# Performance work log

Hardware: AMD Instinct MI355X
Metric: run time of the kernel (lower is better)

Reference implementation:

```python
import jax, jax.numpy as jnp
import numpy as np
from jax import lax

BATCH, SEQ_LEN, HIDDEN, CLASSES = 512, 256, 1024, 128

def _xavier(key, shape):
    fan_out, fan_in = shape
    std = float(np.sqrt(2.0 / (fan_in + fan_out)))
    return jax.random.normal(key, shape, dtype=jnp.float32) * std

def setup_inputs() -> dict:
    key = jax.random.key(0)
    k_x, k_hx, k_hh, k_ph = jax.random.split(key, 4)
    return {
        "x": jax.random.normal(k_x, (BATCH, SEQ_LEN), dtype=jnp.float32),
        "W_hx": _xavier(k_hx, (HIDDEN, 1)),
        "W_hh": _xavier(k_hh, (HIDDEN, HIDDEN)),
        "b_h": jnp.zeros((HIDDEN,), dtype=jnp.float32),
        "W_ph": _xavier(k_ph, (CLASSES, HIDDEN)),
        "b_p": jnp.zeros((CLASSES,), dtype=jnp.float32),
    }

def reference(x, W_hx, W_hh, b_h, W_ph, b_p):
    # x: [B, T] (input_dim == 1 per timestep, as in the torch module)
    B = x.shape[0]
    H = W_hh.shape[0]
    h0 = jnp.zeros((B, H), dtype=x.dtype)

    def step(h, xt):
        # xt: [B]; xt[:, None] @ W_hx.T -> [B, H]
        h_new = jnp.tanh(xt[:, None] @ W_hx.T + h @ W_hh.T + b_h)
        return h_new, None

    h_last, _ = lax.scan(step, h0, x.T)  # scan over time: x.T is [T, B]
    # Output head applied to final hidden state (loop's last p in torch code)
    return h_last @ W_ph.T + b_p  # [B, num_classes]
```

## Files before the change

### kernel.cpp

```cpp
#include <hip/hip_runtime.h>
#include <stdint.h>


#define BATCH 512
#define SEQ   256
#define HID   1024
#define CLS   128

#define GB 16
#define GJ 16
#define BT 32
#define JT 64
#define WSTR 1028
#define SSTR 1032
#define HSTR 72
#define SMEM_BYTES (JT * WSTR * 2)
#define SS_BYTES   (BT * SSTR * 2)
#define RB_OFF     SS_BYTES
#define HS_OFF     (RB_OFF + 8192)
#define HBUF_HALVES (BATCH * HID)

typedef __attribute__((ext_vector_type(8))) short  bf16x8;
typedef __attribute__((ext_vector_type(4))) short  s16x4;
typedef __attribute__((ext_vector_type(4))) float  f32x4;
typedef __attribute__((ext_vector_type(4))) int    i32x4;
typedef __attribute__((ext_vector_type(2))) unsigned int u32x2;

__device__ __forceinline__ unsigned short f2bf(float f) {
  unsigned int u = __float_as_uint(f);
  u = (u + 0x7FFFu + ((u >> 16) & 1u)) >> 16;
  return (unsigned short)u;
}
__device__ __forceinline__ float b2f(short h) {
  return __uint_as_float(((unsigned int)(unsigned short)h) << 16);
}

__device__ __forceinline__ void store_flag(int* p, int v) {
  asm volatile("global_store_dword %0, %1, off sc0 sc1" :: "v"(p), "v"(v) : "memory");
}
__device__ __forceinline__ int load_flag(const int* p) {
  int v;
  asm volatile("global_load_dword %0, %1, off sc0 sc1\n\t"
               "s_waitcnt vmcnt(0)" : "=v"(v) : "v"(p) : "memory");
  return v;
}
__device__ __forceinline__ void store16(void* p, i32x4 v) {
  asm volatile("global_store_dwordx4 %0, %1, off sc0 sc1" :: "v"(p), "v"(v) : "memory");
}
__device__ __forceinline__ void waitcnt0() {
  asm volatile("s_waitcnt vmcnt(0)" ::: "memory");
}
__device__ __forceinline__ void barrier_lgkm() {
  asm volatile("s_waitcnt lgkmcnt(0)\n\ts_barrier" ::: "memory");
}
__device__ __forceinline__ void issue4(const void* p, i32x4& a, i32x4& b, i32x4& c, i32x4& d) {
  asm volatile(
    "global_load_dwordx4 %0, %4, off sc0 sc1\n\t"
    "global_load_dwordx4 %1, %4, off offset:128 sc0 sc1\n\t"
    "global_load_dwordx4 %2, %4, off offset:256 sc0 sc1\n\t"
    "global_load_dwordx4 %3, %4, off offset:384 sc0 sc1"
    : "=&v"(a), "=&v"(b), "=&v"(c), "=&v"(d)
    : "v"(p) : "memory");
}
#define DEF_WAIT(NAME, N) \
__device__ __forceinline__ void NAME(i32x4& a, i32x4& b, i32x4& c, i32x4& d) { \
  asm volatile("s_waitcnt vmcnt(" #N ")" : "+v"(a), "+v"(b), "+v"(c), "+v"(d) :: "memory"); \
}
DEF_WAIT(wait_vm12, 12)
DEF_WAIT(wait_vm8, 8)
DEF_WAIT(wait_vm4, 4)
DEF_WAIT(wait_vm0, 0)

__device__ __forceinline__ void wr16(short* p, i32x4 v) {
  union { i32x4 i; bf16x8 v8; } u; u.i = v;
  *(bf16x8*)p = u.v8;
}
__device__ __forceinline__ bf16x8 ld8_64(const short* p) {
  union { bf16x8 v8; s16x4 h[2]; } u;
  u.h[0] = *(const s16x4*)p;
  u.h[1] = *(const s16x4*)(p + 4);
  return u.v8;
}
__device__ __forceinline__ float tanh_fast(float z) {
  float e = __expf(2.f * z);
  return 1.f - 2.f / (e + 1.f);
}

template<int CK>
__device__ __forceinline__ void mfma_chunk(const short* sA0, const bf16x8 (&fB)[2][16],
                                           f32x4 (&acc)[2][2]) {
#pragma unroll
  for (int ks = 0; ks < 8; ++ks) {
    const int kk = CK * 8 + ks;
    bf16x8 a0 = *(const bf16x8*)(sA0 + CK * 256 + ks * 32);
    bf16x8 a1 = *(const bf16x8*)(sA0 + 16 * SSTR + CK * 256 + ks * 32);
#pragma unroll
    for (int nt = 0; nt < 2; ++nt) {
      acc[0][nt] = __builtin_amdgcn_mfma_f32_16x16x32_bf16(a0, fB[nt][kk], acc[0][nt], 0, 0, 0);
      acc[1][nt] = __builtin_amdgcn_mfma_f32_16x16x32_bf16(a1, fB[nt][kk], acc[1][nt], 0, 0, 0);
    }
  }
}

__global__ void __launch_bounds__(256, 1)
rnn_persistent(const float* __restrict__ x, const float* __restrict__ Whx,
               const float* __restrict__ Whh, const float* __restrict__ bh,
               const float* __restrict__ Wph, const float* __restrict__ bp,
               float* __restrict__ out, unsigned short* hbuf, int* flags)
{
  extern __shared__ short smem[];
  short* sW   = smem;
  short* sS   = smem;
  float* rbuf = (float*)((char*)smem + RB_OFF);
  short* hS   = (short*)((char*)smem + HS_OFF);

  const int tid  = threadIdx.x;
  const int bg   = blockIdx.x & 15;
  const int jg   = blockIdx.x >> 4;
  const int lane = tid & 63;
  const int wv   = tid >> 6;
  const int l15  = lane & 15;
  const int quad = lane >> 4;
  const int npair = wv & 1;
  const int khalf = wv >> 1;

  {
    const int jr = tid >> 2;
    const int kq = tid & 3;
    const float* src = Whh + (jg * JT + jr) * HID + kq * 256;
    short* dst = sW + jr * WSTR + kq * 256;
#pragma unroll 4
    for (int i = 0; i < 64; ++i) {
      float4 f = *(const float4*)(src + i * 4);
      s16x4 h4;
      h4.x = (short)f2bf(f.x); h4.y = (short)f2bf(f.y);
      h4.z = (short)f2bf(f.z); h4.w = (short)f2bf(f.w);
      *(s16x4*)(dst + i * 4) = h4;
    }
  }
  __syncthreads();

  bf16x8 fB[2][16];
#pragma unroll
  for (int nt = 0; nt < 2; ++nt) {
    const short* bp_ = sW + (npair * 32 + nt * 16 + l15) * WSTR + khalf * 512 + quad * 8;
#pragma unroll
    for (int kk = 0; kk < 16; ++kk)
      fB[nt][kk] = ld8_64(bp_ + kk * 32);
  }
  __syncthreads();

  const int jbase = jg * JT + npair * 32;
  const float whx0 = Whx[jbase + l15];
  const float whx1 = Whx[jbase + 16 + l15];
  const float bh0  = bh[jbase + l15];
  const float bh1  = bh[jbase + 16 + l15];

  const int sr  = tid >> 3;
  const int seg = tid & 7;

  int* myflags = flags + bg * 64;

  const short* sA0 = sS + l15 * SSTR + khalf * 512 + quad * 8;

  for (int t = 0; t < SEQ; ++t) {
    const unsigned short* hin = hbuf + ((t + 1) & 1) * HBUF_HALVES;
    unsigned short*      hout = hbuf + (t & 1) * HBUF_HALVES;

    f32x4 acc[2][2];
#pragma unroll
    for (int mt = 0; mt < 2; ++mt)
#pragma unroll
      for (int nt = 0; nt < 2; ++nt)
        acc[mt][nt] = (f32x4){0.f, 0.f, 0.f, 0.f};

    float xv[2][4];
    {
      const float* xp = x + (bg * BT + quad * 4) * SEQ + t;
#pragma unroll
      for (int r = 0; r < 4; ++r) {
        xv[0][r] = xp[r * SEQ];
        xv[1][r] = xp[(16 + r) * SEQ];
      }
    }

    if (t > 0) {
      if (tid < GJ) {
        while (load_flag(myflags + tid) < t) {}
      }
      __syncthreads();

      const char* lbase = (const char*)(hin + (bg * BT + sr) * HID) + seg * 16;
      short* sdst = sS + sr * SSTR + seg * 8;

      i32x4 a0, a1, a2, a3, b0, b1, b2, b3, c0, c1, c2, c3, d0, d1, d2, d3;
      issue4(lbase,        a0, a1, a2, a3);
      issue4(lbase + 512,  b0, b1, b2, b3);
      issue4(lbase + 1024, c0, c1, c2, c3);
      issue4(lbase + 1536, d0, d1, d2, d3);

      wait_vm12(a0, a1, a2, a3);
      wr16(sdst, a0); wr16(sdst + 64, a1); wr16(sdst + 128, a2); wr16(sdst + 192, a3);
      barrier_lgkm();
      if (khalf == 0) mfma_chunk<0>(sA0, fB, acc);

      wait_vm8(b0, b1, b2, b3);
      wr16(sdst + 256, b0); wr16(sdst + 320, b1); wr16(sdst + 384, b2); wr16(sdst + 448, b3);
      barrier_lgkm();
      if (khalf == 0) mfma_chunk<1>(sA0, fB, acc);

      wait_vm4(c0, c1, c2, c3);
      wr16(sdst + 512, c0); wr16(sdst + 576, c1); wr16(sdst + 640, c2); wr16(sdst + 704, c3);
      barrier_lgkm();
      if (khalf == 1) mfma_chunk<0>(sA0, fB, acc);

      wait_vm0(d0, d1, d2, d3);
      wr16(sdst + 768, d0); wr16(sdst + 832, d1); wr16(sdst + 896, d2); wr16(sdst + 960, d3);
      barrier_lgkm();
      if (khalf == 1) mfma_chunk<1>(sA0, fB, acc);
    }

    if (khalf == 1) {
#pragma unroll
      for (int mt = 0; mt < 2; ++mt)
#pragma unroll
        for (int nt = 0; nt < 2; ++nt)
          *(f32x4*)(rbuf + ((npair * 4 + mt * 2 + nt) * 64 + lane) * 4) = acc[mt][nt];
    }
    barrier_lgkm();

    if (khalf == 0) {
#pragma unroll
      for (int mt = 0; mt < 2; ++mt)
#pragma unroll
        for (int nt = 0; nt < 2; ++nt) {
          f32x4 p = *(const f32x4*)(rbuf + ((npair * 4 + mt * 2 + nt) * 64 + lane) * 4);
          acc[mt][nt] += p;
        }
#pragma unroll
      for (int mt = 0; mt < 2; ++mt) {
#pragma unroll
        for (int r = 0; r < 4; ++r) {
          const int row = mt * 16 + quad * 4 + r;
          float z0 = acc[mt][0][r] + xv[mt][r] * whx0 + bh0;
          hS[row * HSTR + npair * 32 + l15] = (short)f2bf(tanh_fast(z0));
          float z1 = acc[mt][1][r] + xv[mt][r] * whx1 + bh1;
          hS[row * HSTR + npair * 32 + 16 + l15] = (short)f2bf(tanh_fast(z1));
        }
      }
    }
    barrier_lgkm();

    {
      union { bf16x8 v8; i32x4 i; } u;
      u.v8 = *(const bf16x8*)(hS + sr * HSTR + seg * 8);
      unsigned short* dst = hout + (bg * BT + sr) * HID + jg * JT + seg * 8;
      store16(dst, u.i);
    }
    waitcnt0();
    barrier_lgkm();
    if (tid == 0) store_flag(myflags + jg, t + 1);
  }

  if (tid < GJ) {
    while (load_flag(myflags + tid) < SEQ) {}
  }
  __syncthreads();

  const unsigned short* hlast = hbuf + ((SEQ - 1) & 1) * HBUF_HALVES;
  {
    const char* lbase = (const char*)(hlast + (bg * BT + sr) * HID) + seg * 16;
    short* sdst = sS + sr * SSTR + seg * 8;
    i32x4 p0, p1, p2, p3;
#pragma unroll
    for (int c = 0; c < 4; ++c) {
      issue4(lbase + c * 512, p0, p1, p2, p3);
      waitcnt0();
      wr16(sdst + c * 256, p0); wr16(sdst + c * 256 + 64, p1);
      wr16(sdst + c * 256 + 128, p2); wr16(sdst + c * 256 + 192, p3);
    }
  }
  __syncthreads();

  const int cc = tid & 7;
  const int cg = jg * 8 + cc;
  const int hr = tid >> 3;
  float acc = 0.f;
  const float* wp = Wph + cg * HID;
  const short* hs = sS + hr * SSTR;
#pragma unroll 8
  for (int k4 = 0; k4 < 256; ++k4) {
    float4 w  = *(const float4*)(wp + k4 * 4);
    s16x4 hv  = *(const s16x4*)(hs + k4 * 4);
    acc += b2f(hv.x) * w.x + b2f(hv.y) * w.y + b2f(hv.z) * w.z + b2f(hv.w) * w.w;
  }
  out[(bg * BT + hr) * CLS + cg] = acc + bp[cg];
}

extern "C" void kernel_launch(void* const* d_in, const int* in_sizes, int n_in,
                              void* d_out, int out_size, void* d_ws, size_t ws_size,
                              hipStream_t stream) {
  const float* x   = (const float*)d_in[0];
  const float* Whx = (const float*)d_in[1];
  const float* Whh = (const float*)d_in[2];
  const float* bh  = (const float*)d_in[3];
  const float* Wph = (const float*)d_in[4];
  const float* bp  = (const float*)d_in[5];
  float* out = (float*)d_out;

  unsigned short* hbuf = (unsigned short*)d_ws;
  int* flags = (int*)((char*)d_ws + (size_t)2 * HBUF_HALVES * 2);

  hipFuncSetAttribute(reinterpret_cast<const void*>(rnn_persistent),
                      hipFuncAttributeMaxDynamicSharedMemorySize, SMEM_BYTES);

  rnn_persistent<<<dim3(GB * GJ), dim3(256), SMEM_BYTES, stream>>>(
      x, Whx, Whh, bh, Wph, bp, out, hbuf, flags);
}
```

Before: 1.147 ms.

## Split batch tile into two half-groups with ping-pong flags to overlap sync

Each block now processes two 16-row batch slices per timestep, A and B, each with its own flag array. While one slice's hidden state is being published and waited on, the other slice's matmul runs, which hides part of the inter-block barrier latency. Operand loads now go straight from global memory into MFMA registers instead of staging through LDS. Flag polling uses a single lane with vectorized min over 16 flags. The cost is more complex dependency ordering and two barriers per half-step.

```diff
diff --git a/kernel.cpp b/kernel.cpp
--- a/kernel.cpp
+++ b/kernel.cpp
@@ -9,22 +9,23 @@
 
 #define GB 16
 #define GJ 16
-#define BT 32
+#define BT 16
 #define JT 64
 #define WSTR 1028
-#define SSTR 1032
 #define HSTR 72
+#define HDSTR 1032
 #define SMEM_BYTES (JT * WSTR * 2)
-#define SS_BYTES   (BT * SSTR * 2)
-#define RB_OFF     SS_BYTES
-#define HS_OFF     (RB_OFF + 8192)
+#define RBA_OFF 0
+#define RBB_OFF 4096
+#define HSA_OFF 8192
+#define HSB_OFF 12288
+#define HEAD_OFF 16384
 #define HBUF_HALVES (BATCH * HID)
 
 typedef __attribute__((ext_vector_type(8))) short  bf16x8;
 typedef __attribute__((ext_vector_type(4))) short  s16x4;
 typedef __attribute__((ext_vector_type(4))) float  f32x4;
 typedef __attribute__((ext_vector_type(4))) int    i32x4;
-typedef __attribute__((ext_vector_type(2))) unsigned int u32x2;
 
 __device__ __forceinline__ unsigned short f2bf(float f) {
   unsigned int u = __float_as_uint(f);
@@ -38,12 +39,6 @@
 __device__ __forceinline__ void store_flag(int* p, int v) {
   asm volatile("global_store_dword %0, %1, off sc0 sc1" :: "v"(p), "v"(v) : "memory");
 }
-__device__ __forceinline__ int load_flag(const int* p) {
-  int v;
-  asm volatile("global_load_dword %0, %1, off sc0 sc1\n\t"
-               "s_waitcnt vmcnt(0)" : "=v"(v) : "v"(p) : "memory");
-  return v;
-}
 __device__ __forceinline__ void store16(void* p, i32x4 v) {
   asm volatile("global_store_dwordx4 %0, %1, off sc0 sc1" :: "v"(p), "v"(v) : "memory");
 }
@@ -53,12 +48,21 @@
 __device__ __forceinline__ void barrier_lgkm() {
   asm volatile("s_waitcnt lgkmcnt(0)\n\ts_barrier" ::: "memory");
 }
-__device__ __forceinline__ void issue4(const void* p, i32x4& a, i32x4& b, i32x4& c, i32x4& d) {
+__device__ __forceinline__ void issue4s(const void* p, i32x4& a, i32x4& b, i32x4& c, i32x4& d) {
   asm volatile(
     "global_load_dwordx4 %0, %4, off sc0 sc1\n\t"
-    "global_load_dwordx4 %1, %4, off offset:128 sc0 sc1\n\t"
-    "global_load_dwordx4 %2, %4, off offset:256 sc0 sc1\n\t"
-    "global_load_dwordx4 %3, %4, off offset:384 sc0 sc1"
+    "global_load_dwordx4 %1, %4, off offset:64 sc0 sc1\n\t"
+    "global_load_dwordx4 %2, %4, off offset:128 sc0 sc1\n\t"
+    "global_load_dwordx4 %3, %4, off offset:192 sc0 sc1"
+    : "=&v"(a), "=&v"(b), "=&v"(c), "=&v"(d)
+    : "v"(p) : "memory");
+}
+__device__ __forceinline__ void issue4c(const void* p, i32x4& a, i32x4& b, i32x4& c, i32x4& d) {
+  asm volatile(
+    "global_load_dwordx4 %0, %4, off sc0 sc1\n\t"
+    "global_load_dwordx4 %1, %4, off offset:16 sc0 sc1\n\t"
+    "global_load_dwordx4 %2, %4, off offset:32 sc0 sc1\n\t"
+    "global_load_dwordx4 %3, %4, off offset:48 sc0 sc1"
     : "=&v"(a), "=&v"(b), "=&v"(c), "=&v"(d)
     : "v"(p) : "memory");
 }
@@ -71,48 +75,54 @@
 DEF_WAIT(wait_vm4, 4)
 DEF_WAIT(wait_vm0, 0)
 
-__device__ __forceinline__ void wr16(short* p, i32x4 v) {
-  union { i32x4 i; bf16x8 v8; } u; u.i = v;
-  *(bf16x8*)p = u.v8;
-}
-__device__ __forceinline__ bf16x8 ld8_64(const short* p) {
-  union { bf16x8 v8; s16x4 h[2]; } u;
-  u.h[0] = *(const s16x4*)p;
-  u.h[1] = *(const s16x4*)(p + 4);
-  return u.v8;
-}
+__device__ __forceinline__ int flags_min16(const int* p) {
+  i32x4 f0, f1, f2, f3;
+  asm volatile(
+    "global_load_dwordx4 %0, %4, off sc0 sc1\n\t"
+    "global_load_dwordx4 %1, %4, off offset:16 sc0 sc1\n\t"
+    "global_load_dwordx4 %2, %4, off offset:32 sc0 sc1\n\t"
+    "global_load_dwordx4 %3, %4, off offset:48 sc0 sc1\n\t"
+    "s_waitcnt vmcnt(0)"
+    : "=&v"(f0), "=&v"(f1), "=&v"(f2), "=&v"(f3) : "v"(p) : "memory");
+  int m = f0.x;
+  m = f0.y < m ? f0.y : m;  m = f0.z < m ? f0.z : m;  m = f0.w < m ? f0.w : m;
+  m = f1.x < m ? f1.x : m;  m = f1.y < m ? f1.y : m;  m = f1.z < m ? f1.z : m;  m = f1.w < m ? f1.w : m;
+  m = f2.x < m ? f2.x : m;  m = f2.y < m ? f2.y : m;  m = f2.z < m ? f2.z : m;  m = f2.w < m ? f2.w : m;
+  m = f3.x < m ? f3.x : m;  m = f3.y < m ? f3.y : m;  m = f3.z < m ? f3.z : m;  m = f3.w < m ? f3.w : m;
+  return m;
+}
+__device__ __forceinline__ void wave_spin(const int* p, int t, int lane) {
+  if (lane == 0) {
+    while (flags_min16(p) < t) {}
+  }
+}
+
 __device__ __forceinline__ float tanh_fast(float z) {
   float e = __expf(2.f * z);
   return 1.f - 2.f / (e + 1.f);
 }
 
-template<int CK>
-__device__ __forceinline__ void mfma_chunk(const short* sA0, const bf16x8 (&fB)[2][16],
-                                           f32x4 (&acc)[2][2]) {
-#pragma unroll
-  for (int ks = 0; ks < 8; ++ks) {
-    const int kk = CK * 8 + ks;
-    bf16x8 a0 = *(const bf16x8*)(sA0 + CK * 256 + ks * 32);
-    bf16x8 a1 = *(const bf16x8*)(sA0 + 16 * SSTR + CK * 256 + ks * 32);
-#pragma unroll
-    for (int nt = 0; nt < 2; ++nt) {
-      acc[0][nt] = __builtin_amdgcn_mfma_f32_16x16x32_bf16(a0, fB[nt][kk], acc[0][nt], 0, 0, 0);
-      acc[1][nt] = __builtin_amdgcn_mfma_f32_16x16x32_bf16(a1, fB[nt][kk], acc[1][nt], 0, 0, 0);
-    }
-  }
+__device__ __forceinline__ void mfma2(i32x4 av, bf16x8 fb0, bf16x8 fb1,
+                                      f32x4& acc0, f32x4& acc1) {
+  union { i32x4 i; bf16x8 v8; } u; u.i = av;
+  acc0 = __builtin_amdgcn_mfma_f32_16x16x32_bf16(u.v8, fb0, acc0, 0, 0, 0);
+  acc1 = __builtin_amdgcn_mfma_f32_16x16x32_bf16(u.v8, fb1, acc1, 0, 0, 0);
 }
 
 __global__ void __launch_bounds__(256, 1)
 rnn_persistent(const float* __restrict__ x, const float* __restrict__ Whx,
                const float* __restrict__ Whh, const float* __restrict__ bh,
                const float* __restrict__ Wph, const float* __restrict__ bp,
-               float* __restrict__ out, unsigned short* hbuf, int* flags)
+               float* __restrict__ out, unsigned short* hbuf,
+               int* flagsA, int* flagsB)
 {
   extern __shared__ short smem[];
   short* sW   = smem;
-  short* sS   = smem;
-  float* rbuf = (float*)((char*)smem + RB_OFF);
-  short* hS   = (short*)((char*)smem + HS_OFF);
+  float* rbA  = (float*)((char*)smem + RBA_OFF);
+  float* rbB  = (float*)((char*)smem + RBB_OFF);
+  short* hSA  = (short*)((char*)smem + HSA_OFF);
+  short* hSB  = (short*)((char*)smem + HSB_OFF);
+  short* hd   = (short*)((char*)smem + HEAD_OFF);
 
   const int tid  = threadIdx.x;
   const int bg   = blockIdx.x & 15;
@@ -145,156 +155,201 @@
   for (int nt = 0; nt < 2; ++nt) {
     const short* bp_ = sW + (npair * 32 + nt * 16 + l15) * WSTR + khalf * 512 + quad * 8;
 #pragma unroll
-    for (int kk = 0; kk < 16; ++kk)
-      fB[nt][kk] = ld8_64(bp_ + kk * 32);
+    for (int kk = 0; kk < 16; ++kk) {
+      union { bf16x8 v8; s16x4 h[2]; } u;
+      u.h[0] = *(const s16x4*)(bp_ + kk * 32);
+      u.h[1] = *(const s16x4*)(bp_ + kk * 32 + 4);
+      fB[nt][kk] = u.v8;
+    }
   }
   __syncthreads();
 
-  const int jbase = jg * JT + npair * 32;
-  const float whx0 = Whx[jbase + l15];
-  const float whx1 = Whx[jbase + 16 + l15];
-  const float bh0  = bh[jbase + l15];
-  const float bh1  = bh[jbase + 16 + l15];
-
-  const int sr  = tid >> 3;
-  const int seg = tid & 7;
-
-  int* myflags = flags + bg * 64;
-
-  const short* sA0 = sS + l15 * SSTR + khalf * 512 + quad * 8;
+  const int jb0 = jg * JT + npair * 32;
+  const float whx0 = Whx[jb0 + l15];
+  const float whx1 = Whx[jb0 + 16 + l15];
+  const float bh0  = bh[jb0 + l15];
+  const float bh1  = bh[jb0 + 16 + l15];
+
+  const int browA = bg * BT;
+  const int browB = 256 + bg * BT;
+
+  int* mfA = flagsA + bg * 16;
+  int* mfB = flagsB + bg * 16;
 
   for (int t = 0; t < SEQ; ++t) {
     const unsigned short* hin = hbuf + ((t + 1) & 1) * HBUF_HALVES;
     unsigned short*      hout = hbuf + (t & 1) * HBUF_HALVES;
 
-    f32x4 acc[2][2];
-#pragma unroll
-    for (int mt = 0; mt < 2; ++mt)
-#pragma unroll
-      for (int nt = 0; nt < 2; ++nt)
-        acc[mt][nt] = (f32x4){0.f, 0.f, 0.f, 0.f};
-
-    float xv[2][4];
-    {
-      const float* xp = x + (bg * BT + quad * 4) * SEQ + t;
+    float xv[4];
+    if (khalf == 0) {
+      const float* xp = x + (browA + quad * 4) * SEQ + t;
+#pragma unroll
+      for (int r = 0; r < 4; ++r) xv[r] = xp[r * SEQ];
+    }
+    f32x4 acc0 = {0.f, 0.f, 0.f, 0.f};
+    f32x4 acc1 = {0.f, 0.f, 0.f, 0.f};
+
+    if (t > 0) {
+      const char* ab = (const char*)(hin + (browA + l15) * HID + khalf * 512 + quad * 8);
+      i32x4 a0,a1,a2,a3, b0,b1,b2,b3, c0,c1,c2,c3, d0,d1,d2,d3;
+      issue4s(ab,       a0,a1,a2,a3);
+      issue4s(ab + 256, b0,b1,b2,b3);
+      issue4s(ab + 512, c0,c1,c2,c3);
+      issue4s(ab + 768, d0,d1,d2,d3);
+      wait_vm12(a0,a1,a2,a3);
+      mfma2(a0, fB[0][0],  fB[1][0],  acc0, acc1);
+      mfma2(a1, fB[0][1],  fB[1][1],  acc0, acc1);
+      mfma2(a2, fB[0][2],  fB[1][2],  acc0, acc1);
+      mfma2(a3, fB[0][3],  fB[1][3],  acc0, acc1);
+      wait_vm8(b0,b1,b2,b3);
+      mfma2(b0, fB[0][4],  fB[1][4],  acc0, acc1);
+      mfma2(b1, fB[0][5],  fB[1][5],  acc0, acc1);
+      mfma2(b2, fB[0][6],  fB[1][6],  acc0, acc1);
+      mfma2(b3, fB[0][7],  fB[1][7],  acc0, acc1);
+      wait_vm4(c0,c1,c2,c3);
+      mfma2(c0, fB[0][8],  fB[1][8],  acc0, acc1);
+      mfma2(c1, fB[0][9],  fB[1][9],  acc0, acc1);
+      mfma2(c2, fB[0][10], fB[1][10], acc0, acc1);
+      mfma2(c3, fB[0][11], fB[1][11], acc0, acc1);
+      wait_vm0(d0,d1,d2,d3);
+      mfma2(d0, fB[0][12], fB[1][12], acc0, acc1);
+      mfma2(d1, fB[0][13], fB[1][13], acc0, acc1);
+      mfma2(d2, fB[0][14], fB[1][14], acc0, acc1);
+      mfma2(d3, fB[0][15], fB[1][15], acc0, acc1);
+    }
+    if (khalf == 1) {
+      *(f32x4*)(rbA + ((npair * 2 + 0) * 64 + lane) * 4) = acc0;
+      *(f32x4*)(rbA + ((npair * 2 + 1) * 64 + lane) * 4) = acc1;
+    }
+    barrier_lgkm();
+    if (khalf == 0) {
+      f32x4 p0 = *(const f32x4*)(rbA + ((npair * 2 + 0) * 64 + lane) * 4);
+      f32x4 p1 = *(const f32x4*)(rbA + ((npair * 2 + 1) * 64 + lane) * 4);
+      acc0 += p0; acc1 += p1;
 #pragma unroll
       for (int r = 0; r < 4; ++r) {
-        xv[0][r] = xp[r * SEQ];
-        xv[1][r] = xp[(16 + r) * SEQ];
+        const int row = quad * 4 + r;
+        hSA[row * HSTR + npair * 32 + l15]      = (short)f2bf(tanh_fast(acc0[r] + xv[r] * whx0 + bh0));
+        hSA[row * HSTR + npair * 32 + 16 + l15] = (short)f2bf(tanh_fast(acc1[r] + xv[r] * whx1 + bh1));
       }
     }
+    barrier_lgkm();
+    if (tid < 128) {
+      union { bf16x8 v8; i32x4 i; } u;
+      u.v8 = *(const bf16x8*)(hSA + (tid >> 3) * HSTR + (tid & 7) * 8);
+      store16(hout + (browA + (tid >> 3)) * HID + jg * JT + (tid & 7) * 8, u.i);
+    }
+    if (t > 0) wave_spin(mfB, t, lane);
+    else       waitcnt0();
+    barrier_lgkm();
+    if (tid == 0) store_flag(mfA + jg, t + 1);
+
+    if (khalf == 0) {
+      const float* xp = x + (browB + quad * 4) * SEQ + t;
+#pragma unroll
+      for (int r = 0; r < 4; ++r) xv[r] = xp[r * SEQ];
+    }
+    acc0 = (f32x4){0.f, 0.f, 0.f, 0.f};
+    acc1 = (f32x4){0.f, 0.f, 0.f, 0.f};
 
     if (t > 0) {
-      if (tid < GJ) {
-        while (load_flag(myflags + tid) < t) {}
+      const char* ab = (const char*)(hin + (browB + l15) * HID + khalf * 512 + quad * 8);
+      i32x4 a0,a1,a2,a3, b0,b1,b2,b3, c0,c1,c2,c3, d0,d1,d2,d3;
+      issue4s(ab,       a0,a1,a2,a3);
+      issue4s(ab + 256, b0,b1,b2,b3);
+      issue4s(ab + 512, c0,c1,c2,c3);
+      issue4s(ab + 768, d0,d1,d2,d3);
+      wait_vm12(a0,a1,a2,a3);
+      mfma2(a0, fB[0][0],  fB[1][0],  acc0, acc1);
+      mfma2(a1, fB[0][1],  fB[1][1],  acc0, acc1);
+      mfma2(a2, fB[0][2],  fB[1][2],  acc0, acc1);
+      mfma2(a3, fB[0][3],  fB[1][3],  acc0, acc1);
+      wait_vm8(b0,b1,b2,b3);
+      mfma2(b0, fB[0][4],  fB[1][4],  acc0, acc1);
+      mfma2(b1, fB[0][5],  fB[1][5],  acc0, acc1);
+      mfma2(b2, fB[0][6],  fB[1][6],  acc0, acc1);
+      mfma2(b3, fB[0][7],  fB[1][7],  acc0, acc1);
+      wait_vm4(c0,c1,c2,c3);
+      mfma2(c0, fB[0][8],  fB[1][8],  acc0, acc1);
+      mfma2(c1, fB[0][9],  fB[1][9],  acc0, acc1);
+      mfma2(c2, fB[0][10], fB[1][10], acc0, acc1);
+      mfma2(c3, fB[0][11], fB[1][11], acc0, acc1);
+      wait_vm0(d0,d1,d2,d3);
+      mfma2(d0, fB[0][12], fB[1][12], acc0, acc1);
+      mfma2(d1, fB[0][13], fB[1][13], acc0, acc1);
+      mfma2(d2, fB[0][14], fB[1][14], acc0, acc1);
+      mfma2(d3, fB[0][15], fB[1][15], acc0, acc1);
+    }
+    if (khalf == 1) {
+      *(f32x4*)(rbB + ((npair * 2 + 0) * 64 + lane) * 4) = acc0;
+      *(f32x4*)(rbB + ((npair * 2 + 1) * 64 + lane) * 4) = acc1;
+    }
+    barrier_lgkm();
+    if (khalf == 0) {
+      f32x4 p0 = *(const f32x4*)(rbB + ((npair * 2 + 0) * 64 + lane) * 4);
+      f32x4 p1 = *(const f32x4*)(rbB + ((npair * 2 + 1) * 64 + lane) * 4);
+      acc0 += p0; acc1 += p1;
+#pragma unroll
+      for (int r = 0; r < 4; ++r) {
+        const int row = quad * 4 + r;
+        hSB[row * HSTR + npair * 32 + l15]      = (short)f2bf(tanh_fast(acc0[r] + xv[r] * whx0 + bh0));
+        hSB[row * HSTR + npair * 32 + 16 + l15] = (short)f2bf(tanh_fast(acc1[r] + xv[r] * whx1 + bh1));
       }
-      __syncthreads();
-
-      const char* lbase = (const char*)(hin + (bg * BT + sr) * HID) + seg * 16;
-      short* sdst = sS + sr * SSTR + seg * 8;
-
-      i32x4 a0, a1, a2, a3, b0, b1, b2, b3, c0, c1, c2, c3, d0, d1, d2, d3;
-      issue4(lbase,        a0, a1, a2, a3);
-      issue4(lbase + 512,  b0, b1, b2, b3);
-      issue4(lbase + 1024, c0, c1, c2, c3);
-      issue4(lbase + 1536, d0, d1, d2, d3);
-
-      wait_vm12(a0, a1, a2, a3);
-      wr16(sdst, a0); wr16(sdst + 64, a1); wr16(sdst + 128, a2); wr16(sdst + 192, a3);
-      barrier_lgkm();
-      if (khalf == 0) mfma_chunk<0>(sA0, fB, acc);
-
-      wait_vm8(b0, b1, b2, b3);
-      wr16(sdst + 256, b0); wr16(sdst + 320, b1); wr16(sdst + 384, b2); wr16(sdst + 448, b3);
-      barrier_lgkm();
-      if (khalf == 0) mfma_chunk<1>(sA0, fB, acc);
-
-      wait_vm4(c0, c1, c2, c3);
-      wr16(sdst + 512, c0); wr16(sdst + 576, c1); wr16(sdst + 640, c2); wr16(sdst + 704, c3);
-      barrier_lgkm();
-      if (khalf == 1) mfma_chunk<0>(sA0, fB, acc);
-
-      wait_vm0(d0, d1, d2, d3);
-      wr16(sdst + 768, d0); wr16(sdst + 832, d1); wr16(sdst + 896, d2); wr16(sdst + 960, d3);
-      barrier_lgkm();
-      if (khalf == 1) mfma_chunk<1>(sA0, fB, acc);
-    }
-
-    if (khalf == 1) {
-#pragma unroll
-      for (int mt = 0; mt < 2; ++mt)
-#pragma unroll
-        for (int nt = 0; nt < 2; ++nt)
-          *(f32x4*)(rbuf + ((npair * 4 + mt * 2 + nt) * 64 + lane) * 4) = acc[mt][nt];
-    }
-    barrier_lgkm();
-
-    if (khalf == 0) {
-#pragma unroll
-      for (int mt = 0; mt < 2; ++mt)
-#pragma unroll
-        for (int nt = 0; nt < 2; ++nt) {
-          f32x4 p = *(const f32x4*)(rbuf + ((npair * 4 + mt * 2 + nt) * 64 + lane) * 4);
-          acc[mt][nt] += p;
-        }
-#pragma unroll
-      for (int mt = 0; mt < 2; ++mt) {
-#pragma unroll
-        for (int r = 0; r < 4; ++r) {
-          const int row = mt * 16 + quad * 4 + r;
-          float z0 = acc[mt][0][r] + xv[mt][r] * whx0 + bh0;
-          hS[row * HSTR + npair * 32 + l15] = (short)f2bf(tanh_fast(z0));
-          float z1 = acc[mt][1][r] + xv[mt][r] * whx1 + bh1;
-          hS[row * HSTR + npair * 32 + 16 + l15] = (short)f2bf(tanh_fast(z1));
-        }
-      }
-    }
-    barrier_lgkm();
-
-    {
+    }
+    barrier_lgkm();
+    if (tid < 128) {
       union { bf16x8 v8; i32x4 i; } u;
-      u.v8 = *(const bf16x8*)(hS + sr * HSTR + seg * 8);
-      unsigned short* dst = hout + (bg * BT + sr) * HID + jg * JT + seg * 8;
-      store16(dst, u.i);
-    }
-    waitcnt0();
-    barrier_lgkm();
-    if (tid == 0) store_flag(myflags + jg, t + 1);
-  }
-
-  if (tid < GJ) {
-    while (load_flag(myflags + tid) < SEQ) {}
-  }
-  __syncthreads();
+      u.v8 = *(const bf16x8*)(hSB + (tid >> 3) * HSTR + (tid & 7) * 8);
+      store16(hout + (browB + (tid >> 3)) * HID + jg * JT + (tid & 7) * 8, u.i);
+    }
+    wave_spin(mfA, t + 1, lane);
+    barrier_lgkm();
+    if (tid == 0) store_flag(mfB + jg, t + 1);
+  }
+
+  wave_spin(mfB, SEQ, lane);
+  barrier_lgkm();
 
   const unsigned short* hlast = hbuf + ((SEQ - 1) & 1) * HBUF_HALVES;
   {
-    const char* lbase = (const char*)(hlast + (bg * BT + sr) * HID) + seg * 16;
-    short* sdst = sS + sr * SSTR + seg * 8;
-    i32x4 p0, p1, p2, p3;
-#pragma unroll
-    for (int c = 0; c < 4; ++c) {
-      issue4(lbase + c * 512, p0, p1, p2, p3);
-      waitcnt0();
-      wr16(sdst + c * 256, p0); wr16(sdst + c * 256 + 64, p1);
-      wr16(sdst + c * 256 + 128, p2); wr16(sdst + c * 256 + 192, p3);
-    }
+    const int ri  = tid >> 3;
+    const int seg = tid & 7;
+    const int grow = (ri < 16) ? (browA + ri) : (browB + ri - 16);
+    const char* pb = (const char*)(hlast + grow * HID + seg * 128);
+    i32x4 p0,p1,p2,p3, q0,q1,q2,q3, r0,r1,r2,r3, s0,s1,s2,s3;
+    issue4c(pb,       p0,p1,p2,p3);
+    issue4c(pb + 64,  q0,q1,q2,q3);
+    issue4c(pb + 128, r0,r1,r2,r3);
+    issue4c(pb + 192, s0,s1,s2,s3);
+    waitcnt0();
+    short* d = hd + ri * HDSTR + seg * 128;
+    union { i32x4 i; bf16x8 v8; } u;
+    u.i = p0; *(bf16x8*)(d)      = u.v8;  u.i = p1; *(bf16x8*)(d + 8)  = u.v8;
+    u.i = p2; *(bf16x8*)(d + 16) = u.v8;  u.i = p3; *(bf16x8*)(d + 24) = u.v8;
+    u.i = q0; *(bf16x8*)(d + 32) = u.v8;  u.i = q1; *(bf16x8*)(d + 40) = u.v8;
+    u.i = q2; *(bf16x8*)(d + 48) = u.v8;  u.i = q3; *(bf16x8*)(d + 56) = u.v8;
+    u.i = r0; *(bf16x8*)(d + 64) = u.v8;  u.i = r1; *(bf16x8*)(d + 72) = u.v8;
+    u.i = r2; *(bf16x8*)(d + 80) = u.v8;  u.i = r3; *(bf16x8*)(d + 88) = u.v8;
+    u.i = s0; *(bf16x8*)(d + 96) = u.v8;  u.i = s1; *(bf16x8*)(d + 104) = u.v8;
+    u.i = s2; *(bf16x8*)(d + 112) = u.v8; u.i = s3; *(bf16x8*)(d + 120) = u.v8;
   }
   __syncthreads();
-
-  const int cc = tid & 7;
-  const int cg = jg * 8 + cc;
-  const int hr = tid >> 3;
-  float acc = 0.f;
-  const float* wp = Wph + cg * HID;
-  const short* hs = sS + hr * SSTR;
+  {
+    const int ri = tid >> 3;
+    const int cc = tid & 7;
+    const int cg = jg * 8 + cc;
+    const int grow = (ri < 16) ? (browA + ri) : (browB + ri - 16);
+    const float* wp = Wph + cg * HID;
+    const short* hs = hd + ri * HDSTR;
+    float acc = 0.f;
 #pragma unroll 8
-  for (int k4 = 0; k4 < 256; ++k4) {
-    float4 w  = *(const float4*)(wp + k4 * 4);
-    s16x4 hv  = *(const s16x4*)(hs + k4 * 4);
-    acc += b2f(hv.x) * w.x + b2f(hv.y) * w.y + b2f(hv.z) * w.z + b2f(hv.w) * w.w;
-  }
-  out[(bg * BT + hr) * CLS + cg] = acc + bp[cg];
+    for (int k4 = 0; k4 < 256; ++k4) {
+      float4 w = *(const float4*)(wp + k4 * 4);
+      s16x4 hv = *(const s16x4*)(hs + k4 * 4);
+      acc += b2f(hv.x) * w.x + b2f(hv.y) * w.y + b2f(hv.z) * w.z + b2f(hv.w) * w.w;
+    }
+    out[grow * CLS + cg] = acc + bp[cg];
+  }
 }
 
 extern "C" void kernel_launch(void* const* d_in, const int* in_sizes, int n_in,
@@ -309,11 +364,12 @@
   float* out = (float*)d_out;
 
   unsigned short* hbuf = (unsigned short*)d_ws;
-  int* flags = (int*)((char*)d_ws + (size_t)2 * HBUF_HALVES * 2);
+  int* flagsA = (int*)((char*)d_ws + (size_t)2 * HBUF_HALVES * 2);
+  int* flagsB = flagsA + 16 * 16;
 
   hipFuncSetAttribute(reinterpret_cast<const void*>(rnn_persistent),
                       hipFuncAttributeMaxDynamicSharedMemorySize, SMEM_BYTES);
 
   rnn_persistent<<<dim3(GB * GJ), dim3(256), SMEM_BYTES, stream>>>(
-      x, Whx, Whh, bh, Wph, bp, out, hbuf, flags);
-}
+      x, Whx, Whh, bh, Wph, bp, out, hbuf, flagsA, flagsB);
+}
```

After: 1.822 ms. +58.9%, slower.

## Use XCD-local cache scope for h exchange when a batch group shares one XCD

Applied to the files above, without the earlier changes.

At startup each block publishes its XCC_ID, and the blocks of a batch group check whether they all run on the same XCD. If they do, the hidden-state exchange and flag polling use sc0-only (L2-scope) loads and stores instead of sc0 sc1 system-coherent ones, which should cut the round-trip latency per timestep. Flag polling also changes from 16 threads polling one flag each to one thread reading all 16 flags with vector loads and taking the minimum, with a bounded fallback to the coherent path. This adds a startup handshake, and the fast path only runs if the hardware places a group's blocks on one XCD.

```diff
diff --git a/kernel.cpp b/kernel.cpp
--- a/kernel.cpp
+++ b/kernel.cpp
@@ -24,7 +24,6 @@
 typedef __attribute__((ext_vector_type(4))) short  s16x4;
 typedef __attribute__((ext_vector_type(4))) float  f32x4;
 typedef __attribute__((ext_vector_type(4))) int    i32x4;
-typedef __attribute__((ext_vector_type(2))) unsigned int u32x2;
 
 __device__ __forceinline__ unsigned short f2bf(float f) {
   unsigned int u = __float_as_uint(f);
@@ -35,32 +34,86 @@
   return __uint_as_float(((unsigned int)(unsigned short)h) << 16);
 }
 
-__device__ __forceinline__ void store_flag(int* p, int v) {
+template<bool LP>
+__device__ __forceinline__ void g_store_flag(int* p, int v) {
+  if constexpr (LP)
+    asm volatile("global_store_dword %0, %1, off sc0" :: "v"(p), "v"(v) : "memory");
+  else
+    asm volatile("global_store_dword %0, %1, off sc0 sc1" :: "v"(p), "v"(v) : "memory");
+}
+template<bool LP>
+__device__ __forceinline__ void g_store16(void* p, i32x4 v) {
+  if constexpr (LP)
+    asm volatile("global_store_dwordx4 %0, %1, off sc0" :: "v"(p), "v"(v) : "memory");
+  else
+    asm volatile("global_store_dwordx4 %0, %1, off sc0 sc1" :: "v"(p), "v"(v) : "memory");
+}
+template<bool LP>
+__device__ __forceinline__ void g_issue4(const void* p, i32x4& a, i32x4& b, i32x4& c, i32x4& d) {
+  if constexpr (LP)
+    asm volatile(
+      "global_load_dwordx4 %0, %4, off sc0\n\t"
+      "global_load_dwordx4 %1, %4, off offset:128 sc0\n\t"
+      "global_load_dwordx4 %2, %4, off offset:256 sc0\n\t"
+      "global_load_dwordx4 %3, %4, off offset:384 sc0"
+      : "=&v"(a), "=&v"(b), "=&v"(c), "=&v"(d) : "v"(p) : "memory");
+  else
+    asm volatile(
+      "global_load_dwordx4 %0, %4, off sc0 sc1\n\t"
+      "global_load_dwordx4 %1, %4, off offset:128 sc0 sc1\n\t"
+      "global_load_dwordx4 %2, %4, off offset:256 sc0 sc1\n\t"
+      "global_load_dwordx4 %3, %4, off offset:384 sc0 sc1"
+      : "=&v"(a), "=&v"(b), "=&v"(c), "=&v"(d) : "v"(p) : "memory");
+}
+template<bool LP>
+__device__ __forceinline__ int flags_min16(const int* p) {
+  i32x4 f0, f1, f2, f3;
+  if constexpr (LP)
+    asm volatile(
+      "global_load_dwordx4 %0, %4, off sc0\n\t"
+      "global_load_dwordx4 %1, %4, off offset:16 sc0\n\t"
+      "global_load_dwordx4 %2, %4, off offset:32 sc0\n\t"
+      "global_load_dwordx4 %3, %4, off offset:48 sc0\n\t"
+      "s_waitcnt vmcnt(0)"
+      : "=&v"(f0), "=&v"(f1), "=&v"(f2), "=&v"(f3) : "v"(p) : "memory");
+  else
+    asm volatile(
+      "global_load_dwordx4 %0, %4, off sc0 sc1\n\t"
+      "global_load_dwordx4 %1, %4, off offset:16 sc0 sc1\n\t"
+      "global_load_dwordx4 %2, %4, off offset:32 sc0 sc1\n\t"
+      "global_load_dwordx4 %3, %4, off offset:48 sc0 sc1\n\t"
+      "s_waitcnt vmcnt(0)"
+      : "=&v"(f0), "=&v"(f1), "=&v"(f2), "=&v"(f3) : "v"(p) : "memory");
+  int m = f0.x;
+  m = f0.y < m ? f0.y : m;  m = f0.z < m ? f0.z : m;  m = f0.w < m ? f0.w : m;
+  m = f1.x < m ? f1.x : m;  m = f1.y < m ? f1.y : m;  m = f1.z < m ? f1.z : m;  m = f1.w < m ? f1.w : m;
+  m = f2.x < m ? f2.x : m;  m = f2.y < m ? f2.y : m;  m = f2.z < m ? f2.z : m;  m = f2.w < m ? f2.w : m;
+  m = f3.x < m ? f3.x : m;  m = f3.y < m ? f3.y : m;  m = f3.z < m ? f3.z : m;  m = f3.w < m ? f3.w : m;
+  return m;
+}
+__device__ __forceinline__ void flags_minmax16_dev(const int* p, int& mn, int& mx) {
+  i32x4 f0, f1, f2, f3;
+  asm volatile(
+    "global_load_dwordx4 %0, %4, off sc0 sc1\n\t"
+    "global_load_dwordx4 %1, %4, off offset:16 sc0 sc1\n\t"
+    "global_load_dwordx4 %2, %4, off offset:32 sc0 sc1\n\t"
+    "global_load_dwordx4 %3, %4, off offset:48 sc0 sc1\n\t"
+    "s_waitcnt vmcnt(0)"
+    : "=&v"(f0), "=&v"(f1), "=&v"(f2), "=&v"(f3) : "v"(p) : "memory");
+  int a[16] = {f0.x,f0.y,f0.z,f0.w, f1.x,f1.y,f1.z,f1.w,
+               f2.x,f2.y,f2.z,f2.w, f3.x,f3.y,f3.z,f3.w};
+  mn = a[0]; mx = a[0];
+#pragma unroll
+  for (int i = 1; i < 16; ++i) { mn = a[i] < mn ? a[i] : mn; mx = a[i] > mx ? a[i] : mx; }
+}
+__device__ __forceinline__ void store_flag_dev(int* p, int v) {
   asm volatile("global_store_dword %0, %1, off sc0 sc1" :: "v"(p), "v"(v) : "memory");
-}
-__device__ __forceinline__ int load_flag(const int* p) {
-  int v;
-  asm volatile("global_load_dword %0, %1, off sc0 sc1\n\t"
-               "s_waitcnt vmcnt(0)" : "=v"(v) : "v"(p) : "memory");
-  return v;
-}
-__device__ __forceinline__ void store16(void* p, i32x4 v) {
-  asm volatile("global_store_dwordx4 %0, %1, off sc0 sc1" :: "v"(p), "v"(v) : "memory");
 }
 __device__ __forceinline__ void waitcnt0() {
   asm volatile("s_waitcnt vmcnt(0)" ::: "memory");
 }
 __device__ __forceinline__ void barrier_lgkm() {
   asm volatile("s_waitcnt lgkmcnt(0)\n\ts_barrier" ::: "memory");
-}
-__device__ __forceinline__ void issue4(const void* p, i32x4& a, i32x4& b, i32x4& c, i32x4& d) {
-  asm volatile(
-    "global_load_dwordx4 %0, %4, off sc0 sc1\n\t"
-    "global_load_dwordx4 %1, %4, off offset:128 sc0 sc1\n\t"
-    "global_load_dwordx4 %2, %4, off offset:256 sc0 sc1\n\t"
-    "global_load_dwordx4 %3, %4, off offset:384 sc0 sc1"
-    : "=&v"(a), "=&v"(b), "=&v"(c), "=&v"(d)
-    : "v"(p) : "memory");
 }
 #define DEF_WAIT(NAME, N) \
 __device__ __forceinline__ void NAME(i32x4& a, i32x4& b, i32x4& c, i32x4& d) { \
@@ -75,12 +128,6 @@
   union { i32x4 i; bf16x8 v8; } u; u.i = v;
   *(bf16x8*)p = u.v8;
 }
-__device__ __forceinline__ bf16x8 ld8_64(const short* p) {
-  union { bf16x8 v8; s16x4 h[2]; } u;
-  u.h[0] = *(const s16x4*)p;
-  u.h[1] = *(const s16x4*)(p + 4);
-  return u.v8;
-}
 __device__ __forceinline__ float tanh_fast(float z) {
   float e = __expf(2.f * z);
   return 1.f - 2.f / (e + 1.f);
@@ -99,6 +146,164 @@
       acc[0][nt] = __builtin_amdgcn_mfma_f32_16x16x32_bf16(a0, fB[nt][kk], acc[0][nt], 0, 0, 0);
       acc[1][nt] = __builtin_amdgcn_mfma_f32_16x16x32_bf16(a1, fB[nt][kk], acc[1][nt], 0, 0, 0);
     }
+  }
+}
+
+template<bool LP>
+__device__ __forceinline__ void spin_flags(const int* myflags, int t) {
+  if constexpr (LP) {
+    int tries = 0;
+    for (;;) {
+      if (flags_min16<true>(myflags) >= t) return;
+      if (++tries >= 64) break;
+    }
+    while (flags_min16<false>(myflags) < t) {}
+  } else {
+    while (flags_min16<false>(myflags) < t) {}
+  }
+}
+
+template<bool LP>
+__device__ __forceinline__ void rnn_body(
+    const float* __restrict__ x, const float* __restrict__ Wph,
+    const float* __restrict__ bp, float* __restrict__ out,
+    unsigned short* hbuf, int* myflags,
+    short* sS, float* rbuf, short* hS,
+    const bf16x8 (&fB)[2][16],
+    int tid, int bg, int jg, int lane, int npair, int khalf,
+    int l15, int quad,
+    float whx0, float whx1, float bh0, float bh1,
+    int sr, int seg)
+{
+  const short* sA0 = sS + l15 * SSTR + khalf * 512 + quad * 8;
+
+  for (int t = 0; t < SEQ; ++t) {
+    const unsigned short* hin = hbuf + ((t + 1) & 1) * HBUF_HALVES;
+    unsigned short*      hout = hbuf + (t & 1) * HBUF_HALVES;
+
+    f32x4 acc[2][2];
+#pragma unroll
+    for (int mt = 0; mt < 2; ++mt)
+#pragma unroll
+      for (int nt = 0; nt < 2; ++nt)
+        acc[mt][nt] = (f32x4){0.f, 0.f, 0.f, 0.f};
+
+    float xv[2][4];
+    {
+      const float* xp = x + (bg * BT + quad * 4) * SEQ + t;
+#pragma unroll
+      for (int r = 0; r < 4; ++r) {
+        xv[0][r] = xp[r * SEQ];
+        xv[1][r] = xp[(16 + r) * SEQ];
+      }
+    }
+
+    if (t > 0) {
+      if (tid == 0) spin_flags<LP>(myflags, t);
+      __syncthreads();
+
+      const char* lbase = (const char*)(hin + (bg * BT + sr) * HID) + seg * 16;
+      short* sdst = sS + sr * SSTR + seg * 8;
+
+      i32x4 a0, a1, a2, a3, b0, b1, b2, b3, c0, c1, c2, c3, d0, d1, d2, d3;
+      g_issue4<LP>(lbase,        a0, a1, a2, a3);
+      g_issue4<LP>(lbase + 512,  b0, b1, b2, b3);
+      g_issue4<LP>(lbase + 1024, c0, c1, c2, c3);
+      g_issue4<LP>(lbase + 1536, d0, d1, d2, d3);
+
+      wait_vm12(a0, a1, a2, a3);
+      wr16(sdst, a0); wr16(sdst + 64, a1); wr16(sdst + 128, a2); wr16(sdst + 192, a3);
+      barrier_lgkm();
+      if (khalf == 0) mfma_chunk<0>(sA0, fB, acc);
+
+      wait_vm8(b0, b1, b2, b3);
+      wr16(sdst + 256, b0); wr16(sdst + 320, b1); wr16(sdst + 384, b2); wr16(sdst + 448, b3);
+      barrier_lgkm();
+      if (khalf == 0) mfma_chunk<1>(sA0, fB, acc);
+
+      wait_vm4(c0, c1, c2, c3);
+      wr16(sdst + 512, c0); wr16(sdst + 576, c1); wr16(sdst + 640, c2); wr16(sdst + 704, c3);
+      barrier_lgkm();
+      if (khalf == 1) mfma_chunk<0>(sA0, fB, acc);
+
+      wait_vm0(d0, d1, d2, d3);
+      wr16(sdst + 768, d0); wr16(sdst + 832, d1); wr16(sdst + 896, d2); wr16(sdst + 960, d3);
+      barrier_lgkm();
+      if (khalf == 1) mfma_chunk<1>(sA0, fB, acc);
+    }
+
+    if (khalf == 1) {
+#pragma unroll
+      for (int mt = 0; mt < 2; ++mt)
+#pragma unroll
+        for (int nt = 0; nt < 2; ++nt)
+          *(f32x4*)(rbuf + ((npair * 4 + mt * 2 + nt) * 64 + lane) * 4) = acc[mt][nt];
+    }
+    barrier_lgkm();
+
+    if (khalf == 0) {
+#pragma unroll
+      for (int mt = 0; mt < 2; ++mt)
+#pragma unroll
+        for (int nt = 0; nt < 2; ++nt) {
+          f32x4 p = *(const f32x4*)(rbuf + ((npair * 4 + mt * 2 + nt) * 64 + lane) * 4);
+          acc[mt][nt] += p;
+        }
+#pragma unroll
+      for (int mt = 0; mt < 2; ++mt) {
+#pragma unroll
+        for (int r = 0; r < 4; ++r) {
+          const int row = mt * 16 + quad * 4 + r;
+          float z0 = acc[mt][0][r] + xv[mt][r] * whx0 + bh0;
+          hS[row * HSTR + npair * 32 + l15] = (short)f2bf(tanh_fast(z0));
+          float z1 = acc[mt][1][r] + xv[mt][r] * whx1 + bh1;
+          hS[row * HSTR + npair * 32 + 16 + l15] = (short)f2bf(tanh_fast(z1));
+        }
+      }
+    }
+    barrier_lgkm();
+
+    {
+      union { bf16x8 v8; i32x4 i; } u;
+      u.v8 = *(const bf16x8*)(hS + sr * HSTR + seg * 8);
+      g_store16<LP>(hout + (bg * BT + sr) * HID + jg * JT + seg * 8, u.i);
+    }
+    waitcnt0();
+    barrier_lgkm();
+    if (tid == 0) g_store_flag<LP>(myflags + jg, t + 1);
+  }
+
+  if (tid == 0) spin_flags<LP>(myflags, SEQ);
+  __syncthreads();
+
+  const unsigned short* hlast = hbuf + ((SEQ - 1) & 1) * HBUF_HALVES;
+  {
+    const char* lbase = (const char*)(hlast + (bg * BT + sr) * HID) + seg * 16;
+    short* sdst = sS + sr * SSTR + seg * 8;
+    i32x4 p0, p1, p2, p3;
+#pragma unroll
+    for (int c = 0; c < 4; ++c) {
+      g_issue4<LP>(lbase + c * 512, p0, p1, p2, p3);
+      waitcnt0();
+      wr16(sdst + c * 256, p0); wr16(sdst + c * 256 + 64, p1);
+      wr16(sdst + c * 256 + 128, p2); wr16(sdst + c * 256 + 192, p3);
+    }
+  }
+  __syncthreads();
+
+  {
+    const int cg = jg * 8 + (tid & 7);
+    const int hr = tid >> 3;
+    float acc = 0.f;
+    const float* wp = Wph + cg * HID;
+    const short* hs = sS + hr * SSTR;
+#pragma unroll 8
+    for (int k4 = 0; k4 < 256; ++k4) {
+      float4 w  = *(const float4*)(wp + k4 * 4);
+      s16x4 hv  = *(const s16x4*)(hs + k4 * 4);
+      acc += b2f(hv.x) * w.x + b2f(hv.y) * w.y + b2f(hv.z) * w.z + b2f(hv.w) * w.w;
+    }
+    out[(bg * BT + hr) * CLS + cg] = acc + bp[cg];
   }
 }
 
@@ -113,6 +318,7 @@
   short* sS   = smem;
   float* rbuf = (float*)((char*)smem + RB_OFF);
   short* hS   = (short*)((char*)smem + HS_OFF);
+  __shared__ int s_local;
 
   const int tid  = threadIdx.x;
   const int bg   = blockIdx.x & 15;
@@ -123,6 +329,15 @@
   const int quad = lane >> 4;
   const int npair = wv & 1;
   const int khalf = wv >> 1;
+
+  int* myflags = flags + bg * 64;
+  int* xline   = myflags + 16;
+
+  if (tid == 0) {
+    int xcd;
+    asm volatile("s_getreg_b32 %0, hwreg(HW_REG_XCC_ID)" : "=s"(xcd));
+    store_flag_dev(xline + jg, 4096 + xcd);
+  }
 
   {
     const int jr = tid >> 2;
@@ -145,156 +360,38 @@
   for (int nt = 0; nt < 2; ++nt) {
     const short* bp_ = sW + (npair * 32 + nt * 16 + l15) * WSTR + khalf * 512 + quad * 8;
 #pragma unroll
-    for (int kk = 0; kk < 16; ++kk)
-      fB[nt][kk] = ld8_64(bp_ + kk * 32);
+    for (int kk = 0; kk < 16; ++kk) {
+      union { bf16x8 v8; s16x4 h[2]; } u;
+      u.h[0] = *(const s16x4*)(bp_ + kk * 32);
+      u.h[1] = *(const s16x4*)(bp_ + kk * 32 + 4);
+      fB[nt][kk] = u.v8;
+    }
+  }
+
+  if (tid == 0) {
+    int mn, mx;
+    do { flags_minmax16_dev(xline, mn, mx); } while (mn < 4096);
+    s_local = (mn == mx) ? 1 : 0;
   }
   __syncthreads();
-
-  const int jbase = jg * JT + npair * 32;
-  const float whx0 = Whx[jbase + l15];
-  const float whx1 = Whx[jbase + 16 + l15];
-  const float bh0  = bh[jbase + l15];
-  const float bh1  = bh[jbase + 16 + l15];
-
+  const bool local = (s_local != 0);
+
+  const int jb0 = jg * JT + npair * 32;
+  const float whx0 = Whx[jb0 + l15];
+  const float whx1 = Whx[jb0 + 16 + l15];
+  const float bh0  = bh[jb0 + l15];
+  const float bh1  = bh[jb0 + 16 + l15];
   const int sr  = tid >> 3;
   const int seg = tid & 7;
 
-  int* myflags = flags + bg * 64;
-
-  const short* sA0 = sS + l15 * SSTR + khalf * 512 + quad * 8;
-
-  for (int t = 0; t < SEQ; ++t) {
-    const unsigned short* hin = hbuf + ((t + 1) & 1) * HBUF_HALVES;
-    unsigned short*      hout = hbuf + (t & 1) * HBUF_HALVES;
-
-    f32x4 acc[2][2];
-#pragma unroll
-    for (int mt = 0; mt < 2; ++mt)
-#pragma unroll
-      for (int nt = 0; nt < 2; ++nt)
-        acc[mt][nt] = (f32x4){0.f, 0.f, 0.f, 0.f};
-
-    float xv[2][4];
-    {
-      const float* xp = x + (bg * BT + quad * 4) * SEQ + t;
-#pragma unroll
-      for (int r = 0; r < 4; ++r) {
-        xv[0][r] = xp[r * SEQ];
-        xv[1][r] = xp[(16 + r) * SEQ];
-      }
-    }
-
-    if (t > 0) {
-      if (tid < GJ) {
-        while (load_flag(myflags + tid) < t) {}
-      }
-      __syncthreads();
-
-      const char* lbase = (const char*)(hin + (bg * BT + sr) * HID) + seg * 16;
-      short* sdst = sS + sr * SSTR + seg * 8;
-
-      i32x4 a0, a1, a2, a3, b0, b1, b2, b3, c0, c1, c2, c3, d0, d1, d2, d3;
-      issue4(lbase,        a0, a1, a2, a3);
-      issue4(lbase + 512,  b0, b1, b2, b3);
-      issue4(lbase + 1024, c0, c1, c2, c3);
-      issue4(lbase + 1536, d0, d1, d2, d3);
-
-      wait_vm12(a0, a1, a2, a3);
-      wr16(sdst, a0); wr16(sdst + 64, a1); wr16(sdst + 128, a2); wr16(sdst + 192, a3);
-      barrier_lgkm();
-      if (khalf == 0) mfma_chunk<0>(sA0, fB, acc);
-
-      wait_vm8(b0, b1, b2, b3);
-      wr16(sdst + 256, b0); wr16(sdst + 320, b1); wr16(sdst + 384, b2); wr16(sdst + 448, b3);
-      barrier_lgkm();
-      if (khalf == 0) mfma_chunk<1>(sA0, fB, acc);
-
-      wait_vm4(c0, c1, c2, c3);
-      wr16(sdst + 512, c0); wr16(sdst + 576, c1); wr16(sdst + 640, c2); wr16(sdst + 704, c3);
-      barrier_lgkm();
-      if (khalf == 1) mfma_chunk<0>(sA0, fB, acc);
-
-      wait_vm0(d0, d1, d2, d3);
-      wr16(sdst + 768, d0); wr16(sdst + 832, d1); wr16(sdst + 896, d2); wr16(sdst + 960, d3);
-      barrier_lgkm();
-      if (khalf == 1) mfma_chunk<1>(sA0, fB, acc);
-    }
-
-    if (khalf == 1) {
-#pragma unroll
-      for (int mt = 0; mt < 2; ++mt)
-#pragma unroll
-        for (int nt = 0; nt < 2; ++nt)
-          *(f32x4*)(rbuf + ((npair * 4 + mt * 2 + nt) * 64 + lane) * 4) = acc[mt][nt];
-    }
-    barrier_lgkm();
-
-    if (khalf == 0) {
-#pragma unroll
-      for (int mt = 0; mt < 2; ++mt)
-#pragma unroll
-        for (int nt = 0; nt < 2; ++nt) {
-          f32x4 p = *(const f32x4*)(rbuf + ((npair * 4 + mt * 2 + nt) * 64 + lane) * 4);
-          acc[mt][nt] += p;
-        }
-#pragma unroll
-      for (int mt = 0; mt < 2; ++mt) {
-#pragma unroll
-        for (int r = 0; r < 4; ++r) {
-          const int row = mt * 16 + quad * 4 + r;
-          float z0 = acc[mt][0][r] + xv[mt][r] * whx0 + bh0;
-          hS[row * HSTR + npair * 32 + l15] = (short)f2bf(tanh_fast(z0));
-          float z1 = acc[mt][1][r] + xv[mt][r] * whx1 + bh1;
-          hS[row * HSTR + npair * 32 + 16 + l15] = (short)f2bf(tanh_fast(z1));
-        }
-      }
-    }
-    barrier_lgkm();
-
-    {
-      union { bf16x8 v8; i32x4 i; } u;
-      u.v8 = *(const bf16x8*)(hS + sr * HSTR + seg * 8);
-      unsigned short* dst = hout + (bg * BT + sr) * HID + jg * JT + seg * 8;
-      store16(dst, u.i);
-    }
-    waitcnt0();
-    barrier_lgkm();
-    if (tid == 0) store_flag(myflags + jg, t + 1);
-  }
-
-  if (tid < GJ) {
-    while (load_flag(myflags + tid) < SEQ) {}
-  }
-  __syncthreads();
-
-  const unsigned short* hlast = hbuf + ((SEQ - 1) & 1) * HBUF_HALVES;
-  {
-    const char* lbase = (const char*)(hlast + (bg * BT + sr) * HID) + seg * 16;
-    short* sdst = sS + sr * SSTR + seg * 8;
-    i32x4 p0, p1, p2, p3;
-#pragma unroll
-    for (int c = 0; c < 4; ++c) {
-      issue4(lbase + c * 512, p0, p1, p2, p3);
-      waitcnt0();
-      wr16(sdst + c * 256, p0); wr16(sdst + c * 256 + 64, p1);
-      wr16(sdst + c * 256 + 128, p2); wr16(sdst + c * 256 + 192, p3);
-    }
-  }
-  __syncthreads();
-
-  const int cc = tid & 7;
-  const int cg = jg * 8 + cc;
-  const int hr = tid >> 3;
-  float acc = 0.f;
-  const float* wp = Wph + cg * HID;
-  const short* hs = sS + hr * SSTR;
-#pragma unroll 8
-  for (int k4 = 0; k4 < 256; ++k4) {
-    float4 w  = *(const float4*)(wp + k4 * 4);
-    s16x4 hv  = *(const s16x4*)(hs + k4 * 4);
-    acc += b2f(hv.x) * w.x + b2f(hv.y) * w.y + b2f(hv.z) * w.z + b2f(hv.w) * w.w;
-  }
-  out[(bg * BT + hr) * CLS + cg] = acc + bp[cg];
+  if (local)
+    rnn_body<true>(x, Wph, bp, out, hbuf, myflags, sS, rbuf, hS, fB,
+                   tid, bg, jg, lane, npair, khalf, l15, quad,
+                   whx0, whx1, bh0, bh1, sr, seg);
+  else
+    rnn_body<false>(x, Wph, bp, out, hbuf, myflags, sS, rbuf, hS, fB,
+                    tid, bg, jg, lane, npair, khalf, l15, quad,
+                    whx0, whx1, bh0, bh1, sr, seg);
 }
 
 extern "C" void kernel_launch(void* const* d_in, const int* in_sizes, int n_in,
```

Result: slower. 3.823 ms (+233.4%).
